# Optimization experiments

Hardware: AMD Instinct MI355X
Metric: run time of the kernel (lower is better)

The kernel has to match this reference:

```python
import jax, jax.numpy as jnp
import numpy as np

D_MODEL = 1024
N_HEADS = 16
HEAD_DIM = D_MODEL // N_HEADS  # 64, even (required by RoPE)
ROPE_THETA = 10000.0
EPS = 1e-6
PAD_VAL = 1.0


def setup_inputs() -> dict:
    key = jax.random.key(0)
    ks = jax.random.split(key, 5)
    w_scale = 1.0 / np.sqrt(D_MODEL)
    return {
        "x": jax.random.normal(ks[0], (4, 4096, D_MODEL), jnp.float32),
        "Wq": jax.random.normal(ks[1], (D_MODEL, D_MODEL), jnp.float32) * w_scale,
        "Wk": jax.random.normal(ks[2], (D_MODEL, D_MODEL), jnp.float32) * w_scale,
        "Wv": jax.random.normal(ks[3], (D_MODEL, D_MODEL), jnp.float32) * w_scale,
        "Wo": jax.random.normal(ks[4], (D_MODEL, D_MODEL), jnp.float32) * w_scale,
    }


def _rope(x, cos, sin):
    # x: [b, h, s, d]; complex multiply on interleaved (even, odd) pairs,
    # matching torch.view_as_complex on reshape(..., -1, 2).
    x1 = x[..., 0::2]
    x2 = x[..., 1::2]
    r1 = x1 * cos - x2 * sin
    r2 = x1 * sin + x2 * cos
    return jnp.stack([r1, r2], axis=-1).reshape(x.shape)


def reference(x, Wq, Wk, Wv, Wo):
    B, S, D = x.shape
    # qkv projections, split heads -> [b, h, s, hd]
    def split_heads(t):
        return t.reshape(B, S, N_HEADS, HEAD_DIM).transpose(0, 2, 1, 3)
    q = split_heads(x @ Wq)
    k = split_heads(x @ Wk)
    v = split_heads(x @ Wv)

    # precompute_freqs_cis: freqs = 1/theta^(2i/d), angles = t * freqs
    freqs = 1.0 / (ROPE_THETA ** (jnp.arange(0, HEAD_DIM, 2, dtype=jnp.float32) / HEAD_DIM))
    ang = jnp.arange(S, dtype=jnp.float32)[:, None] * freqs[None, :]  # [s, hd/2]
    cos = jnp.cos(ang)[None, None]  # [1,1,s,hd/2]
    sin = jnp.sin(ang)[None, None]
    q = _rope(q, cos, sin)
    k = _rope(k, cos, sin)

    # linear_attn_op: ReLU feature maps + padded-value normalization trick
    q = jax.nn.relu(q)
    k = jax.nn.relu(k)
    v_pad = jnp.pad(v, ((0, 0), (0, 0), (0, 0), (0, 1)), constant_values=PAD_VAL)
    # vk: [b, h, d+1, d] -- tiny state, linear complexity in seq
    vk = jnp.einsum('bhke,bhkd->bhed', v_pad, k)
    num = jnp.einsum('bhed,bhld->bhle', vk, q)  # [b, h, s, d+1]
    attn = num[..., :-1] / (num[..., -1:] + EPS)  # [b, h, s, d]

    out = attn.transpose(0, 2, 1, 3).reshape(B, S, D)
    return out @ Wo
```

## Files before the change

kernel.cpp:

```cpp
#include <hip/hip_runtime.h>
#include <stdint.h>

#define GLOBAL_AS __attribute__((address_space(1)))
#define LDS_AS __attribute__((address_space(3)))

typedef float f32x4 __attribute__((ext_vector_type(4)));
typedef short bf16x8 __attribute__((ext_vector_type(8)));

static __device__ __forceinline__ unsigned short f2b(float f) {
  union { float f; unsigned u; } v; v.f = f;
  return (unsigned short)((v.u + 0x7FFFu + ((v.u >> 16) & 1u)) >> 16);
}

static __device__ __forceinline__ void async16(const void* g, void* l) {
  __builtin_amdgcn_global_load_lds((const GLOBAL_AS unsigned int*)g,
                                   (LDS_AS unsigned int*)l, 16, 0, 0);
}

__global__ void prep_kernel(const float* __restrict__ x,
                            const float* __restrict__ Wq, const float* __restrict__ Wk,
                            const float* __restrict__ Wv, const float* __restrict__ Wo,
                            unsigned short* __restrict__ xb,
                            unsigned short* __restrict__ WcatT, unsigned short* __restrict__ WoT,
                            float* __restrict__ cosT, float* __restrict__ sinT) {
  __shared__ float tile[32][33];
  const int bid = blockIdx.x;
  const int tid = threadIdx.x;
  if (bid < 16384) {
    const int i = bid * 256 + tid;
    float4 v = ((const float4*)x)[i];
    ushort4 o;
    o.x = f2b(v.x); o.y = f2b(v.y); o.z = f2b(v.z); o.w = f2b(v.w);
    ((ushort4*)xb)[i] = o;
  } else if (bid < 16384 + 512) {
    const int idx = (bid - 16384) * 256 + tid;
    const int s = idx >> 5, j = idx & 31;
    float freq = expf(-((float)(2 * j) * (1.0f / 64.0f)) * 9.210340371976184f);
    float ang = (float)s * freq;
    float sn, cs;
    sincosf(ang, &sn, &cs);
    cosT[idx] = cs;
    sinT[idx] = sn;
  } else {
    const int t = bid - 16896;
    const int mat = t >> 10;
    const int r = t & 1023;
    const int k0 = (r & 31) * 32, n0 = (r >> 5) * 32;
    const float* W = (mat == 0) ? Wq : (mat == 1) ? Wk : (mat == 2) ? Wv : Wo;
    unsigned short* WT = (mat < 3) ? (WcatT + (size_t)mat * 1024 * 1024) : WoT;
    const int tx = tid & 31, ty = tid >> 5;
    #pragma unroll
    for (int i = 0; i < 4; i++)
      tile[ty + i * 8][tx] = W[(size_t)(k0 + ty + i * 8) * 1024 + n0 + tx];
    __syncthreads();
    #pragma unroll
    for (int i = 0; i < 4; i++)
      WT[(size_t)(n0 + ty + i * 8) * 1024 + k0 + tx] = f2b(tile[tx][ty + i * 8]);
  }
}

__global__ __launch_bounds__(256, 3)
void gemm_qkv_kernel(const unsigned short* __restrict__ xb,
                     const unsigned short* __restrict__ WT,
                     const float* __restrict__ cosT,
                     const float* __restrict__ sinT,
                     unsigned short* __restrict__ Qd,
                     unsigned short* __restrict__ KTd,
                     unsigned short* __restrict__ VTd) {
  __shared__ char sA[16384];
  __shared__ char sB[16384];
  const int tid = threadIdx.x;
  const int lane = tid & 63;
  const int wave = tid >> 6;
  const int lrow = lane & 15;
  const int quad = lane >> 4;
  const int m0 = blockIdx.x * 128;
  const int n0 = blockIdx.y * 128;
  const int wrow = (wave >> 1) * 64;
  const int wcol = (wave & 1) * 64;

  const f32x4 zf = {0.f, 0.f, 0.f, 0.f};
  f32x4 acc[4][4];
  #pragma unroll
  for (int i = 0; i < 4; i++)
    #pragma unroll
    for (int j = 0; j < 4; j++) acc[i][j] = zf;

  const int srow = tid >> 3;
  const int gcol = ((tid & 7) ^ (srow & 7)) * 8;

  for (int kt = 0; kt < 1024; kt += 64) {
    __syncthreads();
    #pragma unroll
    for (int i = 0; i < 4; i++) {
      async16(xb + (size_t)(m0 + i * 32 + srow) * 1024 + kt + gcol, &sA[i * 4096 + tid * 16]);
      async16(WT + (size_t)(n0 + i * 32 + srow) * 1024 + kt + gcol, &sB[i * 4096 + tid * 16]);
    }
    __syncthreads();
    #pragma unroll
    for (int kk = 0; kk < 2; kk++) {
      const int kc = kk * 4 + quad;
      bf16x8 af[4], bfr[4];
      #pragma unroll
      for (int mt = 0; mt < 4; mt++) {
        const int row = wrow + mt * 16 + lrow;
        af[mt] = *(const bf16x8*)&sA[row * 128 + ((kc ^ (row & 7)) << 4)];
      }
      #pragma unroll
      for (int nt = 0; nt < 4; nt++) {
        const int row = wcol + nt * 16 + lrow;
        bfr[nt] = *(const bf16x8*)&sB[row * 128 + ((kc ^ (row & 7)) << 4)];
      }
      #pragma unroll
      for (int mt = 0; mt < 4; mt++)
        #pragma unroll
        for (int nt = 0; nt < 4; nt++)
          acc[mt][nt] = __builtin_amdgcn_mfma_f32_16x16x32_bf16(af[mt], bfr[nt], acc[mt][nt], 0, 0, 0);
    }
  }

  const int b = m0 >> 12;
  const int sec = n0 >> 10;
  const int s0 = (m0 & 4095) + wrow;
  const int c0 = (n0 & 1023) + wcol;

  if (sec == 2) {
    #pragma unroll
    for (int mt = 0; mt < 4; mt++) {
      const int sB4 = s0 + mt * 16 + quad * 4;
      #pragma unroll
      for (int nt = 0; nt < 4; nt++) {
        const int c = c0 + nt * 16 + lrow;
        const int h = c >> 6, e = c & 63;
        ushort4 pk;
        pk.x = f2b(acc[mt][nt][0]); pk.y = f2b(acc[mt][nt][1]);
        pk.z = f2b(acc[mt][nt][2]); pk.w = f2b(acc[mt][nt][3]);
        *(ushort4*)&VTd[((size_t)(b * 16 + h) * 64 + e) * 4096 + sB4] = pk;
      }
    }
  } else {
    #pragma unroll
    for (int mt = 0; mt < 4; mt++) {
      const int sB4 = s0 + mt * 16 + quad * 4;
      #pragma unroll
      for (int nt = 0; nt < 4; nt++) {
        const int c = c0 + nt * 16 + lrow;
        const int j = (c & 63) >> 1;
        float ov[4];
        #pragma unroll
        for (int r = 0; r < 4; r++) {
          const float v = acc[mt][nt][r];
          const float p = __shfl_xor(v, 1, 64);
          const int s = sB4 + r;
          const float cs = cosT[s * 32 + j];
          const float sn = sinT[s * 32 + j];
          const float t = (lane & 1) ? p * sn : -p * sn;
          ov[r] = fmaxf(fmaf(v, cs, t), 0.0f);
        }
        if (sec == 0) {
          const int grow = m0 + wrow + mt * 16 + quad * 4;
          #pragma unroll
          for (int r = 0; r < 4; r++)
            Qd[(size_t)(grow + r) * 1024 + c] = f2b(ov[r]);
        } else {
          const int h = c >> 6, d = c & 63;
          ushort4 pk;
          pk.x = f2b(ov[0]); pk.y = f2b(ov[1]); pk.z = f2b(ov[2]); pk.w = f2b(ov[3]);
          *(ushort4*)&KTd[((size_t)(b * 16 + h) * 64 + d) * 4096 + sB4] = pk;
        }
      }
    }
  }
}

__global__ __launch_bounds__(256)
void vk_partial_kernel(const unsigned short* __restrict__ KTd,
                       const unsigned short* __restrict__ VTd,
                       float* __restrict__ vkp) {
  __shared__ char sV[4096];
  __shared__ char sK[4096];
  const int tid = threadIdx.x;
  const int lane = tid & 63;
  const int wave = tid >> 6;
  const int lrow = lane & 15;
  const int quad = lane >> 4;
  const int bh = blockIdx.x;
  const int kb = blockIdx.y;
  const int s00 = kb * 512;

  const f32x4 zf = {0.f, 0.f, 0.f, 0.f};
  f32x4 acc[5];
  #pragma unroll
  for (int i = 0; i < 5; i++) acc[i] = zf;

  bf16x8 af4;
  const short oneb = (short)0x3F80;
  #pragma unroll
  for (int j = 0; j < 8; j++) af4[j] = (lrow == 0) ? oneb : (short)0;

  const int srow = tid >> 2;
  const int gcol = ((tid & 3) ^ (srow & 3)) * 8;

  for (int kt = 0; kt < 512; kt += 32) {
    __syncthreads();
    async16(VTd + ((size_t)bh * 64 + srow) * 4096 + s00 + kt + gcol, &sV[tid * 16]);
    async16(KTd + ((size_t)bh * 64 + srow) * 4096 + s00 + kt + gcol, &sK[tid * 16]);
    __syncthreads();
    const int rowK = wave * 16 + lrow;
    bf16x8 bfrag = *(const bf16x8*)&sK[rowK * 64 + ((quad ^ (rowK & 3)) << 4)];
    #pragma unroll
    for (int mt = 0; mt < 4; mt++) {
      const int rowV = mt * 16 + lrow;
      bf16x8 af = *(const bf16x8*)&sV[rowV * 64 + ((quad ^ (rowV & 3)) << 4)];
      acc[mt] = __builtin_amdgcn_mfma_f32_16x16x32_bf16(af, bfrag, acc[mt], 0, 0, 0);
    }
    acc[4] = __builtin_amdgcn_mfma_f32_16x16x32_bf16(af4, bfrag, acc[4], 0, 0, 0);
  }

  #pragma unroll
  for (int mt = 0; mt < 5; mt++) {
    #pragma unroll
    for (int r = 0; r < 4; r++) {
      const int e = mt * 16 + quad * 4 + r;
      const int d = wave * 16 + lrow;
      vkp[((size_t)(bh * 8 + kb) * 80 + e) * 64 + d] = acc[mt][r];
    }
  }
}

__global__ void vk_reduce_kernel(const float* __restrict__ vkp, unsigned short* __restrict__ vkb) {
  int idx = blockIdx.x * 256 + threadIdx.x;
  if (idx >= 64 * 80 * 64) return;
  int bh = idx / 5120, r = idx % 5120;
  float s = 0.f;
  #pragma unroll
  for (int kb = 0; kb < 8; kb++) s += vkp[(size_t)(bh * 8 + kb) * 5120 + r];
  vkb[idx] = f2b(s);
}

__global__ __launch_bounds__(256)
void attn_kernel(const unsigned short* __restrict__ Qd,
                 const unsigned short* __restrict__ vkb,
                 unsigned short* __restrict__ attn) {
  __shared__ char sQ[32768];
  __shared__ char sVK[10240];
  const int tid = threadIdx.x;
  const int lane = tid & 63;
  const int wave = tid >> 6;
  const int lrow = lane & 15;
  const int quad = lane >> 4;
  const int bh = blockIdx.y, b = bh >> 4, h = bh & 15;
  const int l0 = b * 4096 + blockIdx.x * 256;

  const int c4 = tid & 7;
  #pragma unroll
  for (int r = 0; r < 8; r++) {
    const int o = r * 4096 + tid * 16;
    const int row = o >> 7;
    const int g4 = c4 ^ (row & 7);
    async16(Qd + (size_t)(l0 + row) * 1024 + h * 64 + g4 * 8, &sQ[o]);
  }
  {
    int row = tid >> 3;
    int g4 = c4 ^ (row & 7);
    async16(vkb + (size_t)bh * 5120 + row * 64 + g4 * 8, &sVK[tid * 16]);
    row += 32; g4 = c4 ^ (row & 7);
    async16(vkb + (size_t)bh * 5120 + row * 64 + g4 * 8, &sVK[4096 + tid * 16]);
    if (tid < 128) {
      row = 64 + (tid >> 3); g4 = c4 ^ (row & 7);
      async16(vkb + (size_t)bh * 5120 + row * 64 + g4 * 8, &sVK[8192 + tid * 16]);
    }
  }
  __syncthreads();

  const f32x4 zf = {0.f, 0.f, 0.f, 0.f};
  f32x4 acc[4][5];
  #pragma unroll
  for (int i = 0; i < 4; i++)
    #pragma unroll
    for (int j = 0; j < 5; j++) acc[i][j] = zf;

  #pragma unroll
  for (int kk = 0; kk < 2; kk++) {
    const int kc = kk * 4 + quad;
    bf16x8 af[4], bfr[5];
    #pragma unroll
    for (int mt = 0; mt < 4; mt++) {
      const int row = wave * 64 + mt * 16 + lrow;
      af[mt] = *(const bf16x8*)&sQ[row * 128 + ((kc ^ (row & 7)) << 4)];
    }
    #pragma unroll
    for (int nt = 0; nt < 5; nt++) {
      const int row = nt * 16 + lrow;
      bfr[nt] = *(const bf16x8*)&sVK[row * 128 + ((kc ^ (row & 7)) << 4)];
    }
    #pragma unroll
    for (int mt = 0; mt < 4; mt++)
      #pragma unroll
      for (int nt = 0; nt < 5; nt++)
        acc[mt][nt] = __builtin_amdgcn_mfma_f32_16x16x32_bf16(af[mt], bfr[nt], acc[mt][nt], 0, 0, 0);
  }

  #pragma unroll
  for (int mt = 0; mt < 4; mt++) {
    #pragma unroll
    for (int r = 0; r < 4; r++) {
      const float den = __shfl(acc[mt][4][r], lane & 48, 64);
      const float inv = 1.0f / (den + 1e-6f);
      const int l = l0 + wave * 64 + mt * 16 + quad * 4 + r;
      #pragma unroll
      for (int nt = 0; nt < 4; nt++)
        attn[(size_t)l * 1024 + h * 64 + nt * 16 + lrow] = f2b(acc[mt][nt][r] * inv);
    }
  }
}

__global__ __launch_bounds__(256, 3)
void gemm_out_kernel(const unsigned short* __restrict__ A,
                     const unsigned short* __restrict__ BT,
                     float* __restrict__ C) {
  __shared__ char sA[16384];
  __shared__ char sB[16384];
  const int tid = threadIdx.x;
  const int lane = tid & 63;
  const int wave = tid >> 6;
  const int lrow = lane & 15;
  const int quad = lane >> 4;
  const int m0 = blockIdx.x * 128;
  const int n0 = blockIdx.y * 128;
  const int wrow = (wave >> 1) * 64;
  const int wcol = (wave & 1) * 64;

  const f32x4 zf = {0.f, 0.f, 0.f, 0.f};
  f32x4 acc[4][4];
  #pragma unroll
  for (int i = 0; i < 4; i++)
    #pragma unroll
    for (int j = 0; j < 4; j++) acc[i][j] = zf;

  const int srow = tid >> 3;
  const int gcol = ((tid & 7) ^ (srow & 7)) * 8;

  for (int kt = 0; kt < 1024; kt += 64) {
    __syncthreads();
    #pragma unroll
    for (int i = 0; i < 4; i++) {
      async16(A + (size_t)(m0 + i * 32 + srow) * 1024 + kt + gcol, &sA[i * 4096 + tid * 16]);
      async16(BT + (size_t)(n0 + i * 32 + srow) * 1024 + kt + gcol, &sB[i * 4096 + tid * 16]);
    }
    __syncthreads();
    #pragma unroll
    for (int kk = 0; kk < 2; kk++) {
      const int kc = kk * 4 + quad;
      bf16x8 af[4], bfr[4];
      #pragma unroll
      for (int mt = 0; mt < 4; mt++) {
        const int row = wrow + mt * 16 + lrow;
        af[mt] = *(const bf16x8*)&sA[row * 128 + ((kc ^ (row & 7)) << 4)];
      }
      #pragma unroll
      for (int nt = 0; nt < 4; nt++) {
        const int row = wcol + nt * 16 + lrow;
        bfr[nt] = *(const bf16x8*)&sB[row * 128 + ((kc ^ (row & 7)) << 4)];
      }
      #pragma unroll
      for (int mt = 0; mt < 4; mt++)
        #pragma unroll
        for (int nt = 0; nt < 4; nt++)
          acc[mt][nt] = __builtin_amdgcn_mfma_f32_16x16x32_bf16(af[mt], bfr[kk * 0 + nt], acc[mt][nt], 0, 0, 0);
    }
  }

  const int grow = m0 + wrow;
  #pragma unroll
  for (int mt = 0; mt < 4; mt++) {
    #pragma unroll
    for (int nt = 0; nt < 4; nt++) {
      const int c = n0 + wcol + nt * 16 + lrow;
      #pragma unroll
      for (int r = 0; r < 4; r++)
        C[(size_t)(grow + mt * 16 + quad * 4 + r) * 1024 + c] = acc[mt][nt][r];
    }
  }
}

extern "C" void kernel_launch(void* const* d_in, const int* in_sizes, int n_in,
                              void* d_out, int out_size, void* d_ws, size_t ws_size,
                              hipStream_t stream) {
  const float* x  = (const float*)d_in[0];
  const float* Wq = (const float*)d_in[1];
  const float* Wk = (const float*)d_in[2];
  const float* Wv = (const float*)d_in[3];
  const float* Wo = (const float*)d_in[4];
  float* out = (float*)d_out;

  char* ws = (char*)d_ws;
  size_t off = 0;
  auto alloc = [&](size_t bytes) -> char* {
    char* p = ws + off;
    off += (bytes + 255) & ~(size_t)255;
    return p;
  };

  unsigned short* xb    = (unsigned short*)alloc((size_t)16384 * 1024 * 2);
  unsigned short* WcatT = (unsigned short*)alloc((size_t)3072 * 1024 * 2);
  unsigned short* WoT   = (unsigned short*)alloc((size_t)1024 * 1024 * 2);
  float* cosT           = (float*)alloc((size_t)4096 * 32 * 4);
  float* sinT           = (float*)alloc((size_t)4096 * 32 * 4);
  unsigned short* Qd    = (unsigned short*)alloc((size_t)16384 * 1024 * 2);
  unsigned short* KTd   = (unsigned short*)alloc((size_t)64 * 64 * 4096 * 2);
  unsigned short* VTd   = (unsigned short*)alloc((size_t)64 * 64 * 4096 * 2);
  float* vkp            = (float*)alloc((size_t)512 * 5120 * 4);
  unsigned short* vkb   = (unsigned short*)alloc((size_t)64 * 5120 * 2);
  unsigned short* attn  = xb;

  prep_kernel<<<16384 + 512 + 4096, 256, 0, stream>>>(x, Wq, Wk, Wv, Wo, xb, WcatT, WoT, cosT, sinT);
  gemm_qkv_kernel<<<dim3(128, 24), 256, 0, stream>>>(xb, WcatT, cosT, sinT, Qd, KTd, VTd);
  vk_partial_kernel<<<dim3(64, 8), 256, 0, stream>>>(KTd, VTd, vkp);
  vk_reduce_kernel<<<1280, 256, 0, stream>>>(vkp, vkb);
  attn_kernel<<<dim3(16, 64), 256, 0, stream>>>(Qd, vkb, attn);
  gemm_out_kernel<<<dim3(128, 8), 256, 0, stream>>>(attn, WoT, out);
}
```

Before: 314.7 us.

## Triple-buffer GEMM tiles with 256x128 blocks and XCD-aware block swizzle

Both projection GEMMs move to 512-thread blocks computing 256x128 tiles. They use a three-stage async global-to-LDS pipeline with explicit vmcnt waits and raw barriers instead of full syncthreads around each load. A flat block-index swizzle groups tiles across XCDs for L2 reuse, and MFMA sections run at raised priority. The larger LDS footprint (~144KB per block) limits residency to one block per CU, and the per-wave 128x32 tiling increases LDS fragment reads per MFMA.

```diff
diff --git a/kernel.cpp b/kernel.cpp
--- a/kernel.cpp
+++ b/kernel.cpp
@@ -59,7 +59,7 @@
   }
 }
 
-__global__ __launch_bounds__(256, 3)
+__global__ __launch_bounds__(512, 2)
 void gemm_qkv_kernel(const unsigned short* __restrict__ xb,
                      const unsigned short* __restrict__ WT,
                      const float* __restrict__ cosT,
@@ -67,69 +67,103 @@
                      unsigned short* __restrict__ Qd,
                      unsigned short* __restrict__ KTd,
                      unsigned short* __restrict__ VTd) {
-  __shared__ char sA[16384];
-  __shared__ char sB[16384];
+  __shared__ char sA[3][32768];
+  __shared__ char sB[3][16384];
   const int tid = threadIdx.x;
   const int lane = tid & 63;
   const int wave = tid >> 6;
   const int lrow = lane & 15;
   const int quad = lane >> 4;
-  const int m0 = blockIdx.x * 128;
-  const int n0 = blockIdx.y * 128;
-  const int wrow = (wave >> 1) * 64;
-  const int wcol = (wave & 1) * 64;
+  const int wm = wave >> 2;
+  const int wn = wave & 3;
+
+  const int flat = blockIdx.x;
+  const int x = (flat & 7) * 192 + (flat >> 3);
+  const int m0 = (x & 63) * 256;
+  const int n0 = (x >> 6) * 128;
 
   const f32x4 zf = {0.f, 0.f, 0.f, 0.f};
-  f32x4 acc[4][4];
-  #pragma unroll
-  for (int i = 0; i < 4; i++)
-    #pragma unroll
-    for (int j = 0; j < 4; j++) acc[i][j] = zf;
-
-  const int srow = tid >> 3;
-  const int gcol = ((tid & 7) ^ (srow & 7)) * 8;
-
-  for (int kt = 0; kt < 1024; kt += 64) {
-    __syncthreads();
-    #pragma unroll
-    for (int i = 0; i < 4; i++) {
-      async16(xb + (size_t)(m0 + i * 32 + srow) * 1024 + kt + gcol, &sA[i * 4096 + tid * 16]);
-      async16(WT + (size_t)(n0 + i * 32 + srow) * 1024 + kt + gcol, &sB[i * 4096 + tid * 16]);
-    }
-    __syncthreads();
-    #pragma unroll
-    for (int kk = 0; kk < 2; kk++) {
+  f32x4 acc[8][2];
+  #pragma unroll
+  for (int i = 0; i < 8; i++)
+    #pragma unroll
+    for (int j = 0; j < 2; j++) acc[i][j] = zf;
+
+  auto stage = [&](int t, int bi) {
+    const int kt = t * 64;
+    #pragma unroll
+    for (int l = 0; l < 4; ++l) {
+      const int slot = l * 512 + tid;
+      const int row = slot >> 3;
+      const int ch = (slot & 7) ^ (row & 7);
+      async16(xb + (size_t)(m0 + row) * 1024 + kt + ch * 8, &sA[bi][slot * 16]);
+    }
+    #pragma unroll
+    for (int l = 0; l < 2; ++l) {
+      const int slot = l * 512 + tid;
+      const int row = slot >> 3;
+      const int ch = (slot & 7) ^ (row & 7);
+      async16(WT + (size_t)(n0 + row) * 1024 + kt + ch * 8, &sB[bi][slot * 16]);
+    }
+  };
+
+  stage(0, 0);
+  stage(1, 1);
+  asm volatile("s_waitcnt vmcnt(6)" ::: "memory");
+  __builtin_amdgcn_s_barrier();
+  __builtin_amdgcn_sched_barrier(0);
+
+  int cur = 0;
+  #pragma unroll 1
+  for (int t = 0; t < 16; ++t) {
+    if (t < 14) {
+      int nb = cur + 2; if (nb >= 3) nb -= 3;
+      stage(t + 2, nb);
+    }
+    const char* bA = sA[cur];
+    const char* bB = sB[cur];
+    #pragma unroll
+    for (int kk = 0; kk < 2; ++kk) {
       const int kc = kk * 4 + quad;
-      bf16x8 af[4], bfr[4];
-      #pragma unroll
-      for (int mt = 0; mt < 4; mt++) {
-        const int row = wrow + mt * 16 + lrow;
-        af[mt] = *(const bf16x8*)&sA[row * 128 + ((kc ^ (row & 7)) << 4)];
-      }
-      #pragma unroll
-      for (int nt = 0; nt < 4; nt++) {
-        const int row = wcol + nt * 16 + lrow;
-        bfr[nt] = *(const bf16x8*)&sB[row * 128 + ((kc ^ (row & 7)) << 4)];
-      }
-      #pragma unroll
-      for (int mt = 0; mt < 4; mt++)
+      bf16x8 af[8], bfr[2];
+      #pragma unroll
+      for (int nt = 0; nt < 2; ++nt) {
+        const int row = wn * 32 + nt * 16 + lrow;
+        bfr[nt] = *(const bf16x8*)&bB[row * 128 + ((kc ^ (row & 7)) << 4)];
+      }
+      #pragma unroll
+      for (int mt = 0; mt < 8; ++mt) {
+        const int row = wm * 128 + mt * 16 + lrow;
+        af[mt] = *(const bf16x8*)&bA[row * 128 + ((kc ^ (row & 7)) << 4)];
+      }
+      __builtin_amdgcn_s_setprio(1);
+      #pragma unroll
+      for (int mt = 0; mt < 8; ++mt)
         #pragma unroll
-        for (int nt = 0; nt < 4; nt++)
+        for (int nt = 0; nt < 2; ++nt)
           acc[mt][nt] = __builtin_amdgcn_mfma_f32_16x16x32_bf16(af[mt], bfr[nt], acc[mt][nt], 0, 0, 0);
-    }
+      __builtin_amdgcn_s_setprio(0);
+    }
+    if (t < 15) {
+      if (t < 14) { asm volatile("s_waitcnt vmcnt(6)" ::: "memory"); }
+      else        { asm volatile("s_waitcnt vmcnt(0)" ::: "memory"); }
+      __builtin_amdgcn_s_barrier();
+      __builtin_amdgcn_sched_barrier(0);
+    }
+    cur = (cur == 2) ? 0 : cur + 1;
   }
 
   const int b = m0 >> 12;
   const int sec = n0 >> 10;
-  const int s0 = (m0 & 4095) + wrow;
-  const int c0 = (n0 & 1023) + wcol;
+  const int s0 = (m0 & 4095) + wm * 128;
+  const int c0 = (n0 & 1023) + wn * 32;
 
   if (sec == 2) {
     #pragma unroll
-    for (int mt = 0; mt < 4; mt++) {
+    for (int mt = 0; mt < 8; mt++) {
       const int sB4 = s0 + mt * 16 + quad * 4;
       #pragma unroll
-      for (int nt = 0; nt < 4; nt++) {
+      for (int nt = 0; nt < 2; nt++) {
         const int c = c0 + nt * 16 + lrow;
         const int h = c >> 6, e = c & 63;
         ushort4 pk;
@@ -140,10 +174,10 @@
     }
   } else {
     #pragma unroll
-    for (int mt = 0; mt < 4; mt++) {
+    for (int mt = 0; mt < 8; mt++) {
       const int sB4 = s0 + mt * 16 + quad * 4;
       #pragma unroll
-      for (int nt = 0; nt < 4; nt++) {
+      for (int nt = 0; nt < 2; nt++) {
         const int c = c0 + nt * 16 + lrow;
         const int j = (c & 63) >> 1;
         float ov[4];
@@ -154,11 +188,11 @@
           const int s = sB4 + r;
           const float cs = cosT[s * 32 + j];
           const float sn = sinT[s * 32 + j];
-          const float t = (lane & 1) ? p * sn : -p * sn;
-          ov[r] = fmaxf(fmaf(v, cs, t), 0.0f);
+          const float tt = (lane & 1) ? p * sn : -p * sn;
+          ov[r] = fmaxf(fmaf(v, cs, tt), 0.0f);
         }
         if (sec == 0) {
-          const int grow = m0 + wrow + mt * 16 + quad * 4;
+          const int grow = m0 + wm * 128 + mt * 16 + quad * 4;
           #pragma unroll
           for (int r = 0; r < 4; r++)
             Qd[(size_t)(grow + r) * 1024 + c] = f2b(ov[r]);
@@ -315,68 +349,102 @@
   }
 }
 
-__global__ __launch_bounds__(256, 3)
+__global__ __launch_bounds__(512, 2)
 void gemm_out_kernel(const unsigned short* __restrict__ A,
                      const unsigned short* __restrict__ BT,
                      float* __restrict__ C) {
-  __shared__ char sA[16384];
-  __shared__ char sB[16384];
+  __shared__ char sA[3][32768];
+  __shared__ char sB[3][16384];
   const int tid = threadIdx.x;
   const int lane = tid & 63;
   const int wave = tid >> 6;
   const int lrow = lane & 15;
   const int quad = lane >> 4;
-  const int m0 = blockIdx.x * 128;
-  const int n0 = blockIdx.y * 128;
-  const int wrow = (wave >> 1) * 64;
-  const int wcol = (wave & 1) * 64;
+  const int wm = wave >> 2;
+  const int wn = wave & 3;
+
+  const int flat = blockIdx.x;
+  const int x = (flat & 7) * 64 + (flat >> 3);
+  const int m0 = (x & 63) * 256;
+  const int n0 = (x >> 6) * 128;
 
   const f32x4 zf = {0.f, 0.f, 0.f, 0.f};
-  f32x4 acc[4][4];
-  #pragma unroll
-  for (int i = 0; i < 4; i++)
-    #pragma unroll
-    for (int j = 0; j < 4; j++) acc[i][j] = zf;
-
-  const int srow = tid >> 3;
-  const int gcol = ((tid & 7) ^ (srow & 7)) * 8;
-
-  for (int kt = 0; kt < 1024; kt += 64) {
-    __syncthreads();
-    #pragma unroll
-    for (int i = 0; i < 4; i++) {
-      async16(A + (size_t)(m0 + i * 32 + srow) * 1024 + kt + gcol, &sA[i * 4096 + tid * 16]);
-      async16(BT + (size_t)(n0 + i * 32 + srow) * 1024 + kt + gcol, &sB[i * 4096 + tid * 16]);
-    }
-    __syncthreads();
-    #pragma unroll
-    for (int kk = 0; kk < 2; kk++) {
+  f32x4 acc[8][2];
+  #pragma unroll
+  for (int i = 0; i < 8; i++)
+    #pragma unroll
+    for (int j = 0; j < 2; j++) acc[i][j] = zf;
+
+  auto stage = [&](int t, int bi) {
+    const int kt = t * 64;
+    #pragma unroll
+    for (int l = 0; l < 4; ++l) {
+      const int slot = l * 512 + tid;
+      const int row = slot >> 3;
+      const int ch = (slot & 7) ^ (row & 7);
+      async16(A + (size_t)(m0 + row) * 1024 + kt + ch * 8, &sA[bi][slot * 16]);
+    }
+    #pragma unroll
+    for (int l = 0; l < 2; ++l) {
+      const int slot = l * 512 + tid;
+      const int row = slot >> 3;
+      const int ch = (slot & 7) ^ (row & 7);
+      async16(BT + (size_t)(n0 + row) * 1024 + kt + ch * 8, &sB[bi][slot * 16]);
+    }
+  };
+
+  stage(0, 0);
+  stage(1, 1);
+  asm volatile("s_waitcnt vmcnt(6)" ::: "memory");
+  __builtin_amdgcn_s_barrier();
+  __builtin_amdgcn_sched_barrier(0);
+
+  int cur = 0;
+  #pragma unroll 1
+  for (int t = 0; t < 16; ++t) {
+    if (t < 14) {
+      int nb = cur + 2; if (nb >= 3) nb -= 3;
+      stage(t + 2, nb);
+    }
+    const char* bA = sA[cur];
+    const char* bB = sB[cur];
+    #pragma unroll
+    for (int kk = 0; kk < 2; ++kk) {
       const int kc = kk * 4 + quad;
-      bf16x8 af[4], bfr[4];
-      #pragma unroll
-      for (int mt = 0; mt < 4; mt++) {
-        const int row = wrow + mt * 16 + lrow;
-        af[mt] = *(const bf16x8*)&sA[row * 128 + ((kc ^ (row & 7)) << 4)];
-      }
-      #pragma unroll
-      for (int nt = 0; nt < 4; nt++) {
-        const int row = wcol + nt * 16 + lrow;
-        bfr[nt] = *(const bf16x8*)&sB[row * 128 + ((kc ^ (row & 7)) << 4)];
-      }
-      #pragma unroll
-      for (int mt = 0; mt < 4; mt++)
+      bf16x8 af[8], bfr[2];
+      #pragma unroll
+      for (int nt = 0; nt < 2; ++nt) {
+        const int row = wn * 32 + nt * 16 + lrow;
+        bfr[nt] = *(const bf16x8*)&bB[row * 128 + ((kc ^ (row & 7)) << 4)];
+      }
+      #pragma unroll
+      for (int mt = 0; mt < 8; ++mt) {
+        const int row = wm * 128 + mt * 16 + lrow;
+        af[mt] = *(const bf16x8*)&bA[row * 128 + ((kc ^ (row & 7)) << 4)];
+      }
+      __builtin_amdgcn_s_setprio(1);
+      #pragma unroll
+      for (int mt = 0; mt < 8; ++mt)
         #pragma unroll
-        for (int nt = 0; nt < 4; nt++)
-          acc[mt][nt] = __builtin_amdgcn_mfma_f32_16x16x32_bf16(af[mt], bfr[kk * 0 + nt], acc[mt][nt], 0, 0, 0);
-    }
-  }
-
-  const int grow = m0 + wrow;
-  #pragma unroll
-  for (int mt = 0; mt < 4; mt++) {
-    #pragma unroll
-    for (int nt = 0; nt < 4; nt++) {
-      const int c = n0 + wcol + nt * 16 + lrow;
+        for (int nt = 0; nt < 2; ++nt)
+          acc[mt][nt] = __builtin_amdgcn_mfma_f32_16x16x32_bf16(af[mt], bfr[nt], acc[mt][nt], 0, 0, 0);
+      __builtin_amdgcn_s_setprio(0);
+    }
+    if (t < 15) {
+      if (t < 14) { asm volatile("s_waitcnt vmcnt(6)" ::: "memory"); }
+      else        { asm volatile("s_waitcnt vmcnt(0)" ::: "memory"); }
+      __builtin_amdgcn_s_barrier();
+      __builtin_amdgcn_sched_barrier(0);
+    }
+    cur = (cur == 2) ? 0 : cur + 1;
+  }
+
+  const int grow = m0 + wm * 128;
+  #pragma unroll
+  for (int mt = 0; mt < 8; mt++) {
+    #pragma unroll
+    for (int nt = 0; nt < 2; nt++) {
+      const int c = n0 + wn * 32 + nt * 16 + lrow;
       #pragma unroll
       for (int r = 0; r < 4; r++)
         C[(size_t)(grow + mt * 16 + quad * 4 + r) * 1024 + c] = acc[mt][nt][r];
@@ -415,9 +483,9 @@
   unsigned short* attn  = xb;
 
   prep_kernel<<<16384 + 512 + 4096, 256, 0, stream>>>(x, Wq, Wk, Wv, Wo, xb, WcatT, WoT, cosT, sinT);
-  gemm_qkv_kernel<<<dim3(128, 24), 256, 0, stream>>>(xb, WcatT, cosT, sinT, Qd, KTd, VTd);
+  gemm_qkv_kernel<<<1536, 512, 0, stream>>>(xb, WcatT, cosT, sinT, Qd, KTd, VTd);
   vk_partial_kernel<<<dim3(64, 8), 256, 0, stream>>>(KTd, VTd, vkp);
   vk_reduce_kernel<<<1280, 256, 0, stream>>>(vkp, vkb);
   attn_kernel<<<dim3(16, 64), 256, 0, stream>>>(Qd, vkb, attn);
-  gemm_out_kernel<<<dim3(128, 8), 256, 0, stream>>>(attn, WoT, out);
-}
+  gemm_out_kernel<<<512, 512, 0, stream>>>(attn, WoT, out);
+}
```

After: 404.6 us. 1.29x slower.

## Replace GEMM tiles with 256x256 double-buffered 8-wave pipelined core

Applied to the files above, without the earlier changes.

Both projection GEMMs now share a new core that uses 256x256 output tiles with 512 threads (8 waves). It double-buffers LDS (128 KB), staging the next K-slice in quarter-steps between MFMA groups and tracking completion with explicit vmcnt waits, barriers and setprio. The aim is to hide global-load latency and raise data reuse per tile, replacing the earlier single-buffered 128x128 loop that synced twice per k-step. In exchange it needs large LDS and many registers, which limits occupancy, and the grids get smaller: 768 blocks for QKV and only 256 blocks for the output projection.

```diff
diff --git a/kernel.cpp b/kernel.cpp
--- a/kernel.cpp
+++ b/kernel.cpp
@@ -16,6 +16,8 @@
   __builtin_amdgcn_global_load_lds((const GLOBAL_AS unsigned int*)g,
                                    (LDS_AS unsigned int*)l, 16, 0, 0);
 }
+
+#define BAR() do { __builtin_amdgcn_s_barrier(); __builtin_amdgcn_sched_barrier(0); } while (0)
 
 __global__ void prep_kernel(const float* __restrict__ x,
                             const float* __restrict__ Wq, const float* __restrict__ Wk,
@@ -59,7 +61,145 @@
   }
 }
 
-__global__ __launch_bounds__(256, 3)
+__device__ __forceinline__ void gemm256_core(const unsigned short* __restrict__ Ag,
+                                             const unsigned short* __restrict__ Bg,
+                                             int m0, int n0, char* lds, f32x4 (&acc)[8][4]) {
+  const int tid = threadIdx.x;
+  const int lane = tid & 63;
+  const int lrow = lane & 15;
+  const int quad = lane >> 4;
+  const int wave = tid >> 6;
+  const int wm = wave >> 2;
+  const int wn = wave & 3;
+
+  const unsigned short* Ar0 = Ag + (size_t)m0 * 1024;
+  const unsigned short* Ar1 = Ag + (size_t)(m0 + 128) * 1024;
+  const unsigned short* Br0 = Bg + (size_t)n0 * 1024;
+  const unsigned short* Br1 = Bg + (size_t)(n0 + 128) * 1024;
+
+  auto stage = [&](const unsigned short* src, char* dst) {
+    #pragma unroll
+    for (int l = 0; l < 2; ++l) {
+      const int slot = l * 512 + tid;
+      const int row = slot >> 3;
+      const int ch = (slot & 7) ^ (row & 7);
+      async16(src + (size_t)row * 1024 + ch * 8, dst + slot * 16);
+    }
+  };
+
+  stage(Ar0, lds);
+  stage(Ar1, lds + 16384);
+  stage(Br0, lds + 32768);
+  stage(Br1, lds + 49152);
+  stage(Br0 + 64, lds + 65536 + 32768);
+  stage(Br1 + 64, lds + 65536 + 49152);
+  asm volatile("s_waitcnt vmcnt(4)" ::: "memory");
+  BAR();
+
+  #pragma unroll 1
+  for (int t = 0; t < 16; ++t) {
+    const int kt = t * 64;
+    char* cur = lds + ((t & 1) << 16);
+    char* nxt = lds + (((t + 1) & 1) << 16);
+    const char* aB = cur + wm * 16384;
+    const char* bB = cur + 32768 + (wn >> 1) * 16384;
+    const int br0 = (wn & 1) * 64;
+
+    bf16x8 a[4][2], b01[2][2], b23[2][2];
+
+    #pragma unroll
+    for (int mt = 0; mt < 4; ++mt) {
+      const int r = mt * 16 + lrow;
+      #pragma unroll
+      for (int kk = 0; kk < 2; ++kk) {
+        const int kc = kk * 4 + quad;
+        a[mt][kk] = *(const bf16x8*)(aB + r * 128 + ((kc ^ (r & 7)) << 4));
+      }
+    }
+    #pragma unroll
+    for (int nt = 0; nt < 2; ++nt) {
+      const int r = br0 + nt * 16 + lrow;
+      #pragma unroll
+      for (int kk = 0; kk < 2; ++kk) {
+        const int kc = kk * 4 + quad;
+        b01[nt][kk] = *(const bf16x8*)(bB + r * 128 + ((kc ^ (r & 7)) << 4));
+      }
+    }
+    if (t < 15) stage(Ar0 + kt + 64, nxt);
+    BAR();
+    __builtin_amdgcn_s_setprio(1);
+    #pragma unroll
+    for (int mt = 0; mt < 4; ++mt)
+      #pragma unroll
+      for (int nt = 0; nt < 2; ++nt)
+        #pragma unroll
+        for (int kk = 0; kk < 2; ++kk)
+          acc[mt][nt] = __builtin_amdgcn_mfma_f32_16x16x32_bf16(a[mt][kk], b01[nt][kk], acc[mt][nt], 0, 0, 0);
+    __builtin_amdgcn_s_setprio(0);
+    BAR();
+
+    #pragma unroll
+    for (int nt = 0; nt < 2; ++nt) {
+      const int r = br0 + (nt + 2) * 16 + lrow;
+      #pragma unroll
+      for (int kk = 0; kk < 2; ++kk) {
+        const int kc = kk * 4 + quad;
+        b23[nt][kk] = *(const bf16x8*)(bB + r * 128 + ((kc ^ (r & 7)) << 4));
+      }
+    }
+    if (t < 15) stage(Ar1 + kt + 64, nxt + 16384);
+    BAR();
+    __builtin_amdgcn_s_setprio(1);
+    #pragma unroll
+    for (int mt = 0; mt < 4; ++mt)
+      #pragma unroll
+      for (int nt = 0; nt < 2; ++nt)
+        #pragma unroll
+        for (int kk = 0; kk < 2; ++kk)
+          acc[mt][nt + 2] = __builtin_amdgcn_mfma_f32_16x16x32_bf16(a[mt][kk], b23[nt][kk], acc[mt][nt + 2], 0, 0, 0);
+    __builtin_amdgcn_s_setprio(0);
+    BAR();
+
+    #pragma unroll
+    for (int mt = 0; mt < 4; ++mt) {
+      const int r = 64 + mt * 16 + lrow;
+      #pragma unroll
+      for (int kk = 0; kk < 2; ++kk) {
+        const int kc = kk * 4 + quad;
+        a[mt][kk] = *(const bf16x8*)(aB + r * 128 + ((kc ^ (r & 7)) << 4));
+      }
+    }
+    if (t < 14) stage(Br0 + kt + 128, cur + 32768);
+    BAR();
+    __builtin_amdgcn_s_setprio(1);
+    #pragma unroll
+    for (int mt = 0; mt < 4; ++mt)
+      #pragma unroll
+      for (int nt = 0; nt < 2; ++nt)
+        #pragma unroll
+        for (int kk = 0; kk < 2; ++kk)
+          acc[mt + 4][nt + 2] = __builtin_amdgcn_mfma_f32_16x16x32_bf16(a[mt][kk], b23[nt][kk], acc[mt + 4][nt + 2], 0, 0, 0);
+    __builtin_amdgcn_s_setprio(0);
+    BAR();
+
+    if (t < 14) stage(Br1 + kt + 128, cur + 49152);
+    BAR();
+    __builtin_amdgcn_s_setprio(1);
+    #pragma unroll
+    for (int mt = 0; mt < 4; ++mt)
+      #pragma unroll
+      for (int nt = 0; nt < 2; ++nt)
+        #pragma unroll
+        for (int kk = 0; kk < 2; ++kk)
+          acc[mt + 4][nt] = __builtin_amdgcn_mfma_f32_16x16x32_bf16(a[mt][kk], b01[nt][kk], acc[mt + 4][nt], 0, 0, 0);
+    __builtin_amdgcn_s_setprio(0);
+    if (t < 14)      { asm volatile("s_waitcnt vmcnt(4)" ::: "memory"); }
+    else if (t == 14){ asm volatile("s_waitcnt vmcnt(0)" ::: "memory"); }
+    BAR();
+  }
+}
+
+__global__ __launch_bounds__(512, 2)
 void gemm_qkv_kernel(const unsigned short* __restrict__ xb,
                      const unsigned short* __restrict__ WT,
                      const float* __restrict__ cosT,
@@ -67,100 +207,68 @@
                      unsigned short* __restrict__ Qd,
                      unsigned short* __restrict__ KTd,
                      unsigned short* __restrict__ VTd) {
-  __shared__ char sA[16384];
-  __shared__ char sB[16384];
+  __shared__ char lds[131072];
+  const int m0 = blockIdx.x * 256;
+  const int n0 = blockIdx.y * 256;
+
+  f32x4 acc[8][4];
+  #pragma unroll
+  for (int i = 0; i < 8; ++i)
+    #pragma unroll
+    for (int j = 0; j < 4; ++j) acc[i][j] = (f32x4){0.f, 0.f, 0.f, 0.f};
+
+  gemm256_core(xb, WT, m0, n0, lds, acc);
+
   const int tid = threadIdx.x;
   const int lane = tid & 63;
-  const int wave = tid >> 6;
   const int lrow = lane & 15;
   const int quad = lane >> 4;
-  const int m0 = blockIdx.x * 128;
-  const int n0 = blockIdx.y * 128;
-  const int wrow = (wave >> 1) * 64;
-  const int wcol = (wave & 1) * 64;
-
-  const f32x4 zf = {0.f, 0.f, 0.f, 0.f};
-  f32x4 acc[4][4];
-  #pragma unroll
-  for (int i = 0; i < 4; i++)
-    #pragma unroll
-    for (int j = 0; j < 4; j++) acc[i][j] = zf;
-
-  const int srow = tid >> 3;
-  const int gcol = ((tid & 7) ^ (srow & 7)) * 8;
-
-  for (int kt = 0; kt < 1024; kt += 64) {
-    __syncthreads();
-    #pragma unroll
-    for (int i = 0; i < 4; i++) {
-      async16(xb + (size_t)(m0 + i * 32 + srow) * 1024 + kt + gcol, &sA[i * 4096 + tid * 16]);
-      async16(WT + (size_t)(n0 + i * 32 + srow) * 1024 + kt + gcol, &sB[i * 4096 + tid * 16]);
-    }
-    __syncthreads();
-    #pragma unroll
-    for (int kk = 0; kk < 2; kk++) {
-      const int kc = kk * 4 + quad;
-      bf16x8 af[4], bfr[4];
-      #pragma unroll
-      for (int mt = 0; mt < 4; mt++) {
-        const int row = wrow + mt * 16 + lrow;
-        af[mt] = *(const bf16x8*)&sA[row * 128 + ((kc ^ (row & 7)) << 4)];
-      }
-      #pragma unroll
-      for (int nt = 0; nt < 4; nt++) {
-        const int row = wcol + nt * 16 + lrow;
-        bfr[nt] = *(const bf16x8*)&sB[row * 128 + ((kc ^ (row & 7)) << 4)];
-      }
-      #pragma unroll
-      for (int mt = 0; mt < 4; mt++)
-        #pragma unroll
-        for (int nt = 0; nt < 4; nt++)
-          acc[mt][nt] = __builtin_amdgcn_mfma_f32_16x16x32_bf16(af[mt], bfr[nt], acc[mt][nt], 0, 0, 0);
-    }
-  }
+  const int wave = tid >> 6;
+  const int wm = wave >> 2;
+  const int wn = wave & 3;
 
   const int b = m0 >> 12;
   const int sec = n0 >> 10;
-  const int s0 = (m0 & 4095) + wrow;
-  const int c0 = (n0 & 1023) + wcol;
+  const int s0 = (m0 & 4095) + wm * 128;
+  const int c0 = (n0 & 1023) + wn * 64;
 
   if (sec == 2) {
     #pragma unroll
-    for (int mt = 0; mt < 4; mt++) {
-      const int sB4 = s0 + mt * 16 + quad * 4;
-      #pragma unroll
-      for (int nt = 0; nt < 4; nt++) {
+    for (int i = 0; i < 8; ++i) {
+      const int sB4 = s0 + i * 16 + quad * 4;
+      #pragma unroll
+      for (int nt = 0; nt < 4; ++nt) {
         const int c = c0 + nt * 16 + lrow;
         const int h = c >> 6, e = c & 63;
         ushort4 pk;
-        pk.x = f2b(acc[mt][nt][0]); pk.y = f2b(acc[mt][nt][1]);
-        pk.z = f2b(acc[mt][nt][2]); pk.w = f2b(acc[mt][nt][3]);
+        pk.x = f2b(acc[i][nt][0]); pk.y = f2b(acc[i][nt][1]);
+        pk.z = f2b(acc[i][nt][2]); pk.w = f2b(acc[i][nt][3]);
         *(ushort4*)&VTd[((size_t)(b * 16 + h) * 64 + e) * 4096 + sB4] = pk;
       }
     }
   } else {
     #pragma unroll
-    for (int mt = 0; mt < 4; mt++) {
-      const int sB4 = s0 + mt * 16 + quad * 4;
-      #pragma unroll
-      for (int nt = 0; nt < 4; nt++) {
+    for (int i = 0; i < 8; ++i) {
+      const int sB4 = s0 + i * 16 + quad * 4;
+      #pragma unroll
+      for (int nt = 0; nt < 4; ++nt) {
         const int c = c0 + nt * 16 + lrow;
         const int j = (c & 63) >> 1;
         float ov[4];
         #pragma unroll
-        for (int r = 0; r < 4; r++) {
-          const float v = acc[mt][nt][r];
+        for (int r = 0; r < 4; ++r) {
+          const float v = acc[i][nt][r];
           const float p = __shfl_xor(v, 1, 64);
           const int s = sB4 + r;
           const float cs = cosT[s * 32 + j];
           const float sn = sinT[s * 32 + j];
-          const float t = (lane & 1) ? p * sn : -p * sn;
-          ov[r] = fmaxf(fmaf(v, cs, t), 0.0f);
+          const float tt = (lane & 1) ? p * sn : -p * sn;
+          ov[r] = fmaxf(fmaf(v, cs, tt), 0.0f);
         }
         if (sec == 0) {
-          const int grow = m0 + wrow + mt * 16 + quad * 4;
+          const int grow = m0 + wm * 128 + i * 16 + quad * 4;
           #pragma unroll
-          for (int r = 0; r < 4; r++)
+          for (int r = 0; r < 4; ++r)
             Qd[(size_t)(grow + r) * 1024 + c] = f2b(ov[r]);
         } else {
           const int h = c >> 6, d = c & 63;
@@ -315,71 +423,39 @@
   }
 }
 
-__global__ __launch_bounds__(256, 3)
+__global__ __launch_bounds__(512, 2)
 void gemm_out_kernel(const unsigned short* __restrict__ A,
                      const unsigned short* __restrict__ BT,
                      float* __restrict__ C) {
-  __shared__ char sA[16384];
-  __shared__ char sB[16384];
+  __shared__ char lds[131072];
+  const int m0 = blockIdx.x * 256;
+  const int n0 = blockIdx.y * 256;
+
+  f32x4 acc[8][4];
+  #pragma unroll
+  for (int i = 0; i < 8; ++i)
+    #pragma unroll
+    for (int j = 0; j < 4; ++j) acc[i][j] = (f32x4){0.f, 0.f, 0.f, 0.f};
+
+  gemm256_core(A, BT, m0, n0, lds, acc);
+
   const int tid = threadIdx.x;
   const int lane = tid & 63;
-  const int wave = tid >> 6;
   const int lrow = lane & 15;
   const int quad = lane >> 4;
-  const int m0 = blockIdx.x * 128;
-  const int n0 = blockIdx.y * 128;
-  const int wrow = (wave >> 1) * 64;
-  const int wcol = (wave & 1) * 64;
-
-  const f32x4 zf = {0.f, 0.f, 0.f, 0.f};
-  f32x4 acc[4][4];
-  #pragma unroll
-  for (int i = 0; i < 4; i++)
-    #pragma unroll
-    for (int j = 0; j < 4; j++) acc[i][j] = zf;
-
-  const int srow = tid >> 3;
-  const int gcol = ((tid & 7) ^ (srow & 7)) * 8;
-
-  for (int kt = 0; kt < 1024; kt += 64) {
-    __syncthreads();
-    #pragma unroll
-    for (int i = 0; i < 4; i++) {
-      async16(A + (size_t)(m0 + i * 32 + srow) * 1024 + kt + gcol, &sA[i * 4096 + tid * 16]);
-      async16(BT + (size_t)(n0 + i * 32 + srow) * 1024 + kt + gcol, &sB[i * 4096 + tid * 16]);
-    }
-    __syncthreads();
-    #pragma unroll
-    for (int kk = 0; kk < 2; kk++) {
-      const int kc = kk * 4 + quad;
-      bf16x8 af[4], bfr[4];
-      #pragma unroll
-      for (int mt = 0; mt < 4; mt++) {
-        const int row = wrow + mt * 16 + lrow;
-        af[mt] = *(const bf16x8*)&sA[row * 128 + ((kc ^ (row & 7)) << 4)];
-      }
-      #pragma unroll
-      for (int nt = 0; nt < 4; nt++) {
-        const int row = wcol + nt * 16 + lrow;
-        bfr[nt] = *(const bf16x8*)&sB[row * 128 + ((kc ^ (row & 7)) << 4)];
-      }
-      #pragma unroll
-      for (int mt = 0; mt < 4; mt++)
-        #pragma unroll
-        for (int nt = 0; nt < 4; nt++)
-          acc[mt][nt] = __builtin_amdgcn_mfma_f32_16x16x32_bf16(af[mt], bfr[kk * 0 + nt], acc[mt][nt], 0, 0, 0);
-    }
-  }
-
-  const int grow = m0 + wrow;
-  #pragma unroll
-  for (int mt = 0; mt < 4; mt++) {
-    #pragma unroll
-    for (int nt = 0; nt < 4; nt++) {
-      const int c = n0 + wcol + nt * 16 + lrow;
-      #pragma unroll
-      for (int r = 0; r < 4; r++)
-        C[(size_t)(grow + mt * 16 + quad * 4 + r) * 1024 + c] = acc[mt][nt][r];
+  const int wave = tid >> 6;
+  const int wm = wave >> 2;
+  const int wn = wave & 3;
+
+  const int grow = m0 + wm * 128;
+  #pragma unroll
+  for (int i = 0; i < 8; ++i) {
+    #pragma unroll
+    for (int nt = 0; nt < 4; ++nt) {
+      const int c = n0 + wn * 64 + nt * 16 + lrow;
+      #pragma unroll
+      for (int r = 0; r < 4; ++r)
+        C[(size_t)(grow + i * 16 + quad * 4 + r) * 1024 + c] = acc[i][nt][r];
     }
   }
 }
@@ -415,9 +491,9 @@
   unsigned short* attn  = xb;
 
   prep_kernel<<<16384 + 512 + 4096, 256, 0, stream>>>(x, Wq, Wk, Wv, Wo, xb, WcatT, WoT, cosT, sinT);
-  gemm_qkv_kernel<<<dim3(128, 24), 256, 0, stream>>>(xb, WcatT, cosT, sinT, Qd, KTd, VTd);
+  gemm_qkv_kernel<<<dim3(64, 12), 512, 0, stream>>>(xb, WcatT, cosT, sinT, Qd, KTd, VTd);
   vk_partial_kernel<<<dim3(64, 8), 256, 0, stream>>>(KTd, VTd, vkp);
   vk_reduce_kernel<<<1280, 256, 0, stream>>>(vkp, vkb);
   attn_kernel<<<dim3(16, 64), 256, 0, stream>>>(Qd, vkb, attn);
-  gemm_out_kernel<<<dim3(128, 8), 256, 0, stream>>>(attn, WoT, out);
-}
+  gemm_out_kernel<<<dim3(64, 4), 512, 0, stream>>>(attn, WoT, out);
+}
```

New measurement: 324.0 us. 1.03x slower.
